# Kernel optimization log

Measured on AMD Instinct MI355X. Metric: run time of the kernel, lower is better.

## Reference

```python
import jax, jax.numpy as jnp
import numpy as np

SIGMA = 1.0
DELTA = 1.0
TOPK = 10
TOPK_HALF = 5  # int(np.around(TOPK / 2))


def l2norm(x):
    # F.normalize: x / max(||x||, 1e-12)
    n = jnp.linalg.norm(x, axis=-1, keepdims=True)
    return x / jnp.maximum(n, 1e-12)


def cdist(a, b):
    # pairwise euclidean distance with grad-safe sqrt (0 on exact-zero dists)
    d2 = (jnp.sum(a * a, axis=1)[:, None] + jnp.sum(b * b, axis=1)[None, :]
          - 2.0 * a @ b.T)
    d2 = jnp.maximum(d2, 0.0)
    return jnp.where(d2 > 0.0, jnp.sqrt(jnp.where(d2 > 0.0, d2, 1.0)), 0.0)


def rc_weights(t_emb, idx):
    # all of this is under torch.no_grad() in the original
    N = t_emb.shape[0]
    T_dist = cdist(t_emb, t_emb)
    W_P = jnp.exp(-(T_dist ** 2) / SIGMA)
    same_id = idx[:, None] == idx[None, :]
    W_P_copy = jnp.where(same_id, 1.0, W_P)
    _, topk_index = jax.lax.top_k(W_P_copy, TOPK)            # [N, k]
    topk_half_index = topk_index[:, :TOPK_HALF]               # [N, k/2]
    rows = jnp.arange(N)[:, None]
    W_NN = jnp.zeros((N, N), W_P.dtype).at[rows, topk_index].set(1.0)
    V = (((W_NN + W_NN.T) / 2.0) == 1.0).astype(W_P.dtype)    # mutual-NN graph
    # vectorized form of the per-row loop:
    # W_C_tilda[i, j] = V[i, j] * |N(i) \cap N(j)| / |N(i)|
    deg = V.sum(axis=1)                                       # |N(i)| per row
    VV = V @ V                                                # V symmetric -> (V@V)[i,j] = |N(i) cap N(j)|
    W_C_tilda = jnp.where(V > 0.0, VV / jnp.maximum(deg, 1.0)[:, None], 0.0)
    W_C_hat = W_C_tilda[topk_half_index].mean(axis=1)         # [N, N]
    W_C = (W_C_hat + W_C_hat.T) / 2.0
    W = (W_P + W_C) / 2.0
    off_diag = 1.0 - jnp.eye(N, dtype=W.dtype)
    pos_weight = W * off_diag
    neg_weight = (1.0 - W) * off_diag
    return pos_weight, neg_weight


def rc_loss(s_emb, t_emb, idx):
    s_emb = l2norm(s_emb)        # disable_mu=True
    t_emb = l2norm(t_emb)
    N = s_emb.shape[0]
    S_dist = cdist(s_emb, s_emb)
    S_dist = S_dist / S_dist.mean(axis=1, keepdims=True)
    pos_w, neg_w = rc_weights(t_emb, idx)
    pos_w = jax.lax.stop_gradient(pos_w)
    neg_w = jax.lax.stop_gradient(neg_w)
    pull = jax.nn.relu(S_dist) ** 2 * pos_w
    push = jax.nn.relu(DELTA - S_dist) ** 2 * neg_w
    return (pull.sum() + push.sum()) / (N * (N - 1))


def kl_loss(s_f, s_g):
    # disable_mu=True -> normalize both
    s_f = l2norm(s_f)
    s_g = l2norm(s_g)
    N = s_f.shape[0]
    S_dist = cdist(s_f, s_f)
    S_dist = S_dist / S_dist.mean(axis=1, keepdims=True)
    S_bg = cdist(s_g, s_g)
    S_bg = S_bg / S_bg.mean(axis=1, keepdims=True)
    log_q = jax.nn.log_softmax(-S_dist, axis=-1)
    log_p = jax.nn.log_softmax(jax.lax.stop_gradient(-S_bg), axis=-1)
    p = jnp.exp(log_p)
    return jnp.sum(p * (log_p - log_q)) / N


def setup_inputs() -> dict:
    key = jax.random.key(0)
    k1, k2, k3, k4 = jax.random.split(key, 4)
    N = 4096
    s_f = jax.random.normal(k1, (N, 512), jnp.float32)
    s_g = jax.random.normal(k2, (N, 512), jnp.float32)
    t_g = jax.random.normal(k3, (N, 1024), jnp.float32)
    idx = jax.random.randint(k4, (N,), 0, 2048, jnp.int64 if jax.config.jax_enable_x64 else jnp.int32)
    return {"s_f": s_f, "s_g": s_g, "t_g": t_g, "idx": idx}


def reference(s_f, s_g, t_g, idx):
    loss_RC_f = rc_loss(s_f, t_g, idx)
    loss_RC_g = rc_loss(s_g, t_g, idx)
    loss_RC = (loss_RC_f + loss_RC_g) / 2.0
    loss_KL = kl_loss(s_f, s_g)
    return loss_RC, loss_KL, loss_RC + loss_KL
```

## Files before the change

kernel.cpp:

```cpp
#include <hip/hip_runtime.h>
#include <hip/hip_bf16.h>

#define NN 4096
typedef unsigned short u16;
typedef __bf16 bf16x8 __attribute__((ext_vector_type(8)));
typedef float f32x4 __attribute__((ext_vector_type(4)));
typedef u16 u16x8 __attribute__((ext_vector_type(8)));

typedef const __attribute__((address_space(1))) void* gptr_t;
typedef __attribute__((address_space(3))) void* lptr_t;

__device__ inline u16 bf16bits(float v) {
    __bf16 h = (__bf16)v;
    return __builtin_bit_cast(u16, h);
}
__device__ inline float bf16val(float v) {
    __bf16 h = (__bf16)v;
    return (float)h;
}
__device__ inline float b2f(u16 b) { return __uint_as_float(((unsigned)b) << 16); }

__device__ inline float block_sum(float v, volatile float* sbuf) {
    int lane = threadIdx.x & 63, wv = threadIdx.x >> 6;
#pragma unroll
    for (int o = 32; o > 0; o >>= 1) v += __shfl_xor(v, o, 64);
    if (lane == 0) sbuf[wv] = v;
    __syncthreads();
    float r = sbuf[0] + sbuf[1] + sbuf[2] + sbuf[3];
    __syncthreads();
    return r;
}

template <int D>
__global__ void normalize_kernel(const float* __restrict__ in, u16* __restrict__ outb,
                                 float* __restrict__ ssout) {
    __shared__ float sbuf[4];
    constexpr int NV = D / 4;
    int row = blockIdx.x, tid = threadIdx.x;
    const float4* x4 = (const float4*)(in + (size_t)row * D);
    float4 v = make_float4(0.f, 0.f, 0.f, 0.f);
    if (tid < NV) v = x4[tid];
    float s = v.x * v.x + v.y * v.y + v.z * v.z + v.w * v.w;
    float tot = block_sum(s, sbuf);
    float inv = 1.0f / fmaxf(sqrtf(tot), 1e-12f);
    float sb = 0.f;
    if (tid < NV) {
        float b0 = bf16val(v.x * inv), b1 = bf16val(v.y * inv);
        float b2 = bf16val(v.z * inv), b3 = bf16val(v.w * inv);
        ushort4 o;
        o.x = bf16bits(v.x * inv);
        o.y = bf16bits(v.y * inv);
        o.z = bf16bits(v.z * inv);
        o.w = bf16bits(v.w * inv);
        ((ushort4*)(outb + (size_t)row * D))[tid] = o;
        sb = b0 * b0 + b1 * b1 + b2 * b2 + b3 * b3;
    }
    float totb = block_sum(sb, sbuf);
    if (tid == 0) ssout[row] = totb;
}

#define TS 132
__launch_bounds__(256)
__global__ void gram_merged(const u16* __restrict__ tb, const u16* __restrict__ fb,
                            const u16* __restrict__ gb, const float* __restrict__ ss_t,
                            const float* __restrict__ ss_f, const float* __restrict__ ss_g,
                            u16* __restrict__ WP, u16* __restrict__ Sf, u16* __restrict__ Sg,
                            float* __restrict__ rsf, float* __restrict__ rsg) {
    __shared__ __align__(16) u16 smem[128 * TS];

    int bid = blockIdx.x;
    int which = (bid < 528) ? 0 : (bid < 1056 ? 1 : 2);
    int lb = bid - (which == 0 ? 0 : (which == 1 ? 528 : 1056));
    int by = 0, rem = lb;
    while (rem >= 32 - by) { rem -= 32 - by; ++by; }
    int bx = by + rem;

    const u16* X = (which == 0) ? tb : (which == 1 ? fb : gb);
    const float* ss = (which == 0) ? ss_t : (which == 1 ? ss_f : ss_g);
    u16* outp = (which == 0) ? WP : (which == 1 ? Sf : Sg);
    float* rowsum = (which == 0) ? nullptr : (which == 1 ? rsf : rsg);
    const int K = (which == 0) ? 1024 : 512;
    const bool mode1 = (which != 0);

    const int tid = threadIdx.x;
    const int wv = tid >> 6, lane = tid & 63;
    const int wr = wv >> 1, wc = wv & 1;
    const int brow = by * 128, bcol = bx * 128;
    const int r = lane & 15, kc = lane >> 4;
    const int crow = lane >> 2;
    const int koff = (lane & 3) * 8;

    f32x4 acc[4][4];
#pragma unroll
    for (int mi = 0; mi < 4; ++mi)
#pragma unroll
        for (int ni = 0; ni < 4; ++ni) acc[mi][ni] = (f32x4){0.f, 0.f, 0.f, 0.f};

    auto STAGE = [&](int buf, int k0) {
#pragma unroll
        for (int cc = 0; cc < 2; ++cc) {
            int c = wv * 2 + cc;
            const u16* ga = X + (size_t)(brow + c * 16 + crow) * K + k0 + koff;
            const u16* gbp = X + (size_t)(bcol + c * 16 + crow) * K + k0 + koff;
            __builtin_amdgcn_global_load_lds((gptr_t)ga, (lptr_t)&smem[buf * 4096 + c * 512], 16, 0, 0);
            __builtin_amdgcn_global_load_lds((gptr_t)gbp, (lptr_t)&smem[8192 + buf * 4096 + c * 512], 16, 0, 0);
        }
    };

    const int NT = K / 32;
    STAGE(0, 0);
    __syncthreads();
    for (int t = 0; t < NT; ++t) {
        int cur = t & 1;
        if (t + 1 < NT) STAGE(cur ^ 1, (t + 1) * 32);

        bf16x8 af[4], bfr[4];
#pragma unroll
        for (int mi = 0; mi < 4; ++mi)
            af[mi] = *(const bf16x8*)&smem[cur * 4096 + (wr * 64 + mi * 16 + r) * 32 + kc * 8];
#pragma unroll
        for (int ni = 0; ni < 4; ++ni)
            bfr[ni] = *(const bf16x8*)&smem[8192 + cur * 4096 + (wc * 64 + ni * 16 + r) * 32 + kc * 8];
#pragma unroll
        for (int mi = 0; mi < 4; ++mi)
#pragma unroll
            for (int ni = 0; ni < 4; ++ni)
                acc[mi][ni] = __builtin_amdgcn_mfma_f32_16x16x32_bf16(af[mi], bfr[ni], acc[mi][ni], 0, 0, 0);

        __syncthreads();
    }

    u16* tile = smem;
    const int q = lane >> 4;
#pragma unroll
    for (int mi = 0; mi < 4; ++mi) {
#pragma unroll
        for (int v = 0; v < 4; ++v) {
            int rl = wr * 64 + mi * 16 + q * 4 + v;
            float ssi = ss[brow + rl];
#pragma unroll
            for (int ni = 0; ni < 4; ++ni) {
                int cl = wc * 64 + ni * 16 + r;
                float d2 = fmaxf(ssi + ss[bcol + cl] - 2.0f * acc[mi][ni][v], 0.f);
                float o = mode1 ? sqrtf(d2) : __expf(-d2);
                tile[rl * TS + cl] = bf16bits(o);
            }
        }
    }
    __syncthreads();

    {
        int rl = tid >> 1, hf = tid & 1;
        const u16* srow = &tile[rl * TS + hf * 64];
        u16* drow = outp + (size_t)(brow + rl) * NN + bcol + hf * 64;
        float rs = 0.f;
#pragma unroll
        for (int i = 0; i < 8; ++i) {
            ushort4 aa = *(const ushort4*)(srow + i * 8);
            ushort4 bb = *(const ushort4*)(srow + i * 8 + 4);
            u16x8 pk = {aa.x, aa.y, aa.z, aa.w, bb.x, bb.y, bb.z, bb.w};
            *(u16x8*)(drow + i * 8) = pk;
            if (mode1)
                rs += b2f(aa.x) + b2f(aa.y) + b2f(aa.z) + b2f(aa.w) +
                      b2f(bb.x) + b2f(bb.y) + b2f(bb.z) + b2f(bb.w);
        }
        if (mode1) {
            rs += __shfl_xor(rs, 1, 64);
            if (hf == 0) atomicAdd(&rowsum[brow + rl], rs);
        }
    }

    if (bx != by) {
        int c = tid >> 1, hf = tid & 1;
        u16* drow = outp + (size_t)(bcol + c) * NN + brow + hf * 64;
        float rs = 0.f;
#pragma unroll
        for (int s = 0; s < 8; ++s) {
            u16 g[8];
#pragma unroll
            for (int u = 0; u < 8; ++u) g[u] = tile[(hf * 64 + s * 8 + u) * TS + c];
            u16x8 pk = {g[0], g[1], g[2], g[3], g[4], g[5], g[6], g[7]};
            *(u16x8*)(drow + s * 8) = pk;
            if (mode1)
#pragma unroll
                for (int u = 0; u < 8; ++u) rs += b2f(g[u]);
        }
        if (mode1) {
            rs += __shfl_xor(rs, 1, 64);
            if (hf == 0) atomicAdd(&rowsum[bcol + c], rs);
        }
    }
}

__global__ void topk_kernel(const u16* __restrict__ WP, const int* __restrict__ idx,
                            int* __restrict__ topk) {
    __shared__ unsigned long long sred[4];
    __shared__ unsigned long long sbest;
    int row = blockIdx.x, tid = threadIdx.x;
    int myid = idx[row];
    const u16x8* W8 = (const u16x8*)(WP + (size_t)row * NN);
    const int4* idx4 = (const int4*)idx;
    unsigned key[16];
#pragma unroll
    for (int a = 0; a < 2; ++a) {
        u16x8 w = W8[a * 256 + tid];
        int4 iA = idx4[a * 512 + tid * 2];
        int4 iB = idx4[a * 512 + tid * 2 + 1];
        int ids[8] = {iA.x, iA.y, iA.z, iA.w, iB.x, iB.y, iB.z, iB.w};
#pragma unroll
        for (int c = 0; c < 8; ++c)
            key[a * 8 + c] = (ids[c] == myid) ? 0x3F800000u : (((unsigned)w[c]) << 16);
    }
    int lane = tid & 63, wv = tid >> 6;
    for (int it = 0; it < 10; ++it) {
        unsigned long long best = 0;
#pragma unroll
        for (int a = 0; a < 2; ++a)
#pragma unroll
            for (int c = 0; c < 8; ++c) {
                unsigned j = (unsigned)(a * 2048 + tid * 8 + c);
                unsigned long long pk =
                    ((unsigned long long)key[a * 8 + c] << 32) | (0xFFFFFFFFu - j);
                if (pk > best) best = pk;
            }
#pragma unroll
        for (int o = 32; o > 0; o >>= 1) {
            unsigned long long t = __shfl_xor(best, o, 64);
            if (t > best) best = t;
        }
        if (lane == 0) sred[wv] = best;
        __syncthreads();
        if (tid == 0) {
            unsigned long long b = sred[0];
            for (int w2 = 1; w2 < 4; ++w2)
                if (sred[w2] > b) b = sred[w2];
            sbest = b;
        }
        __syncthreads();
        unsigned jstar = 0xFFFFFFFFu - (unsigned)(sbest & 0xFFFFFFFFu);
        if (tid == 0) topk[row * 10 + it] = (int)jstar;
        if (((jstar >> 3) & 255u) == (unsigned)tid) {
            unsigned slot = ((jstar >> 11) << 3) | (jstar & 7u);
#pragma unroll
            for (int a = 0; a < 16; ++a)
                if ((unsigned)a == slot) key[a] = 0u;
        }
        __syncthreads();
    }
}

__global__ void mutual_kernel(const int* __restrict__ topk, int* __restrict__ nbr,
                              int* __restrict__ deg) {
    int gid = blockIdx.x * 256 + threadIdx.x;
    if (gid >= NN * 10) return;
    int i = gid / 10, a = gid - i * 10;
    int j = topk[i * 10 + a];
    bool mut = false;
#pragma unroll
    for (int b = 0; b < 10; ++b) mut = mut || (topk[j * 10 + b] == i);
    nbr[gid] = mut ? j : -1;
    if (mut) atomicAdd(&deg[i], 1);
}

__global__ void tilda_kernel(const int* __restrict__ nbr, const int* __restrict__ deg,
                             float* __restrict__ tvals) {
    int gid = blockIdx.x * 256 + threadIdx.x;
    if (gid >= NN * 10) return;
    int m = gid / 10;
    int j = nbr[gid];
    if (j < 0) { tvals[gid] = 0.f; return; }
    int am[10], aj[10];
#pragma unroll
    for (int p = 0; p < 10; ++p) am[p] = nbr[m * 10 + p];
#pragma unroll
    for (int p = 0; p < 10; ++p) aj[p] = nbr[j * 10 + p];
    int cnt = 0;
#pragma unroll
    for (int p = 0; p < 10; ++p)
#pragma unroll
        for (int qq = 0; qq < 10; ++qq)
            cnt += (am[p] >= 0 && am[p] == aj[qq]) ? 1 : 0;
    int dm = deg[m];
    float dv = (float)(dm > 1 ? dm : 1);
    tvals[gid] = (float)cnt / dv;
}

__global__ void hat_kernel(const int* __restrict__ topk, const int* __restrict__ nbr,
                           const float* __restrict__ tvals, int* __restrict__ hcols,
                           float* __restrict__ hvals) {
    int gid = blockIdx.x * 256 + threadIdx.x;
    if (gid >= NN * 5) return;
    int i = gid / 5, h = gid - i * 5;
    int m = topk[i * 10 + h];
#pragma unroll
    for (int a = 0; a < 10; ++a) {
        int j = nbr[m * 10 + a];
        int slot = i * 50 + h * 10 + a;
        hcols[slot] = j;
        hvals[slot] = (j >= 0) ? tvals[m * 10 + a] * 0.2f : 0.f;
    }
}

__global__ void fused_dense_kernel(const u16* __restrict__ Sf, const u16* __restrict__ Sg,
                                   const u16* __restrict__ WP, const float* __restrict__ rsf,
                                   const float* __restrict__ rsg, double* __restrict__ acc) {
    __shared__ float sbuf[4];
    int row = blockIdx.x, tid = threadIdx.x;
    float imf = (float)NN / rsf[row];
    float img = (float)NN / rsg[row];
    const u16x8* f8 = (const u16x8*)(Sf + (size_t)row * NN);
    const u16x8* g8 = (const u16x8*)(Sg + (size_t)row * NN);
    const u16x8* w8 = (const u16x8*)(WP + (size_t)row * NN);
    u16x8 fr[2], gr[2];
#pragma unroll
    for (int a = 0; a < 2; ++a) {
        fr[a] = f8[a * 256 + tid];
        gr[a] = g8[a * 256 + tid];
    }
    float vf[16], vg[16];
#pragma unroll
    for (int a = 0; a < 2; ++a)
#pragma unroll
        for (int c = 0; c < 8; ++c) {
            vf[a * 8 + c] = b2f(fr[a][c]) * imf;
            vg[a * 8 + c] = b2f(gr[a][c]) * img;
        }
    float ef = 0.f, eg = 0.f;
#pragma unroll
    for (int a = 0; a < 16; ++a) {
        ef += __expf(-vf[a]);
        eg += __expf(-vg[a]);
    }
    float lf = logf(block_sum(ef, sbuf));
    float lg = logf(block_sum(eg, sbuf));
    u16x8 wr2[2];
#pragma unroll
    for (int a = 0; a < 2; ++a) wr2[a] = w8[a * 256 + tid];
    float af = 0.f, ag = 0.f, akl = 0.f;
#pragma unroll
    for (int a = 0; a < 2; ++a) {
#pragma unroll
        for (int c = 0; c < 8; ++c) {
            int j = a * 2048 + tid * 8 + c;
            float wp = b2f(wr2[a][c]);
            float sf = vf[a * 8 + c], sg = vg[a * 8 + c];
            if (j != row) {
                float t = fmaxf(1.f - sf, 0.f);
                float pu = t * t;
                float gq = sf * sf - pu;
                af += pu + 0.5f * gq * wp;
                t = fmaxf(1.f - sg, 0.f);
                pu = t * t;
                gq = sg * sg - pu;
                ag += pu + 0.5f * gq * wp;
            }
            float lq = -sf - lf;
            float lp = -sg - lg;
            float pp = __expf(lp);
            akl += pp * (lp - lq);
        }
    }
    float tf = block_sum(af, sbuf);
    float tg2 = block_sum(ag, sbuf);
    float tk = block_sum(akl, sbuf);
    if (tid == 0) {
        int bank = (row & 15) * 3;
        atomicAdd(&acc[bank + 0], (double)tf);
        atomicAdd(&acc[bank + 1], (double)tg2);
        atomicAdd(&acc[bank + 2], (double)tk);
    }
}

__global__ void sparse_kernel(const u16* __restrict__ Sf, const u16* __restrict__ Sg,
                              const int* __restrict__ hcols, const float* __restrict__ hvals,
                              const float* __restrict__ rsf, const float* __restrict__ rsg,
                              double* __restrict__ acc) {
    __shared__ float sbuf[4];
    int lane = threadIdx.x & 63, wv = threadIdx.x >> 6;
    int i = blockIdx.x * 4 + wv;
    float cf = 0.f, cg = 0.f;
    if (lane < 50) {
        int j = hcols[i * 50 + lane];
        if (j >= 0 && j != i) {
            float v = hvals[i * 50 + lane];
            float imfi = (float)NN / rsf[i];
            float imgi = (float)NN / rsg[i];
            float s1 = b2f(Sf[(size_t)i * NN + j]) * imfi;
            float s2 = b2f(Sf[(size_t)j * NN + i]) * ((float)NN / rsf[j]);
            float t1 = fmaxf(1.f - s1, 0.f), t2 = fmaxf(1.f - s2, 0.f);
            cf = v * ((s1 * s1 - t1 * t1) + (s2 * s2 - t2 * t2));
            s1 = b2f(Sg[(size_t)i * NN + j]) * imgi;
            s2 = b2f(Sg[(size_t)j * NN + i]) * ((float)NN / rsg[j]);
            t1 = fmaxf(1.f - s1, 0.f);
            t2 = fmaxf(1.f - s2, 0.f);
            cg = v * ((s1 * s1 - t1 * t1) + (s2 * s2 - t2 * t2));
        }
    }
    float tf = block_sum(cf, sbuf);
    float tg = block_sum(cg, sbuf);
    if (threadIdx.x == 0) {
        int bank = (blockIdx.x & 15) * 3;
        atomicAdd(&acc[bank + 0], (double)(0.25f * tf));
        atomicAdd(&acc[bank + 1], (double)(0.25f * tg));
    }
}

__global__ void finalize_kernel(const double* __restrict__ acc, float* __restrict__ out) {
    if (threadIdx.x == 0) {
        double a0 = 0.0, a1 = 0.0, a2 = 0.0;
        for (int b = 0; b < 16; ++b) {
            a0 += acc[b * 3 + 0];
            a1 += acc[b * 3 + 1];
            a2 += acc[b * 3 + 2];
        }
        double denom = (double)NN * (double)(NN - 1);
        double rcf = a0 / denom, rcg = a1 / denom;
        double rc = 0.5 * (rcf + rcg);
        double kl = a2 / (double)NN;
        out[0] = (float)rc;
        out[1] = (float)kl;
        out[2] = (float)(rc + kl);
    }
}

extern "C" void kernel_launch(void* const* d_in, const int* in_sizes, int n_in, void* d_out,
                              int out_size, void* d_ws, size_t ws_size, hipStream_t stream) {
    const float* s_f = (const float*)d_in[0];
    const float* s_g = (const float*)d_in[1];
    const float* t_g = (const float*)d_in[2];
    const int* idx = (const int*)d_in[3];
    float* out = (float*)d_out;

    char* base = (char*)d_ws;
    size_t off = 0;
    auto alloc = [&](size_t b) {
        char* p = base + off;
        off = (off + b + 255) & ~(size_t)255;
        return p;
    };
    double* acc = (double*)alloc(16 * 3 * 8);
    float* rowsum_f = (float*)alloc(NN * 4);
    float* rowsum_g = (float*)alloc(NN * 4);
    int* deg = (int*)alloc(NN * 4);
    size_t zero_bytes = off;
    u16* tb = (u16*)alloc((size_t)NN * 1024 * 2);
    u16* fb = (u16*)alloc((size_t)NN * 512 * 2);
    u16* gb = (u16*)alloc((size_t)NN * 512 * 2);
    float* ss_t = (float*)alloc(NN * 4);
    float* ss_f = (float*)alloc(NN * 4);
    float* ss_g = (float*)alloc(NN * 4);
    u16* WP = (u16*)alloc((size_t)NN * NN * 2);
    u16* Sf = (u16*)alloc((size_t)NN * NN * 2);
    u16* Sg = (u16*)alloc((size_t)NN * NN * 2);
    int* topk = (int*)alloc(NN * 10 * 4);
    int* nbr = (int*)alloc(NN * 10 * 4);
    float* tvals = (float*)alloc(NN * 10 * 4);
    int* hcols = (int*)alloc(NN * 50 * 4);
    float* hvals = (float*)alloc(NN * 50 * 4);

    hipMemsetAsync(d_ws, 0, zero_bytes, stream);

    normalize_kernel<1024><<<NN, 256, 0, stream>>>(t_g, tb, ss_t);
    normalize_kernel<512><<<NN, 256, 0, stream>>>(s_f, fb, ss_f);
    normalize_kernel<512><<<NN, 256, 0, stream>>>(s_g, gb, ss_g);

    gram_merged<<<1584, 256, 0, stream>>>(tb, fb, gb, ss_t, ss_f, ss_g, WP, Sf, Sg,
                                          rowsum_f, rowsum_g);

    topk_kernel<<<NN, 256, 0, stream>>>(WP, idx, topk);
    mutual_kernel<<<(NN * 10 + 255) / 256, 256, 0, stream>>>(topk, nbr, deg);
    tilda_kernel<<<(NN * 10 + 255) / 256, 256, 0, stream>>>(nbr, deg, tvals);
    hat_kernel<<<(NN * 5 + 255) / 256, 256, 0, stream>>>(topk, nbr, tvals, hcols, hvals);

    fused_dense_kernel<<<NN, 256, 0, stream>>>(Sf, Sg, WP, rowsum_f, rowsum_g, acc);
    sparse_kernel<<<NN / 4, 256, 0, stream>>>(Sf, Sg, hcols, hvals, rowsum_f, rowsum_g, acc);
    finalize_kernel<<<1, 64, 0, stream>>>(acc, out);
}
```

Measured before the change: 240.6 us.

## Enlarge gram tiles to 256x256 with 1024-thread blocks and LDS transposed epilogue

The symmetric gram kernel now uses 256x256 output tiles computed by 16 waves in a 1024-thread block, so each tile loads fewer operands relative to its output and the grid drops to 408 blocks. The epilogue writes each 128x128 quadrant through LDS, and off-diagonal tiles also get a transposed copy built in LDS so the mirrored writes are contiguous instead of strided column gathers. The cost is more LDS per block, extra barriers per quadrant, and far fewer blocks, which may leave the GPU's compute units underfilled or unevenly loaded.

```diff
diff --git a/kernel.cpp b/kernel.cpp
--- a/kernel.cpp
+++ b/kernel.cpp
@@ -59,20 +59,20 @@
     if (tid == 0) ssout[row] = totb;
 }
 
-#define TS 132
-__launch_bounds__(256)
+#define TS 136
+__launch_bounds__(1024, 4)
 __global__ void gram_merged(const u16* __restrict__ tb, const u16* __restrict__ fb,
                             const u16* __restrict__ gb, const float* __restrict__ ss_t,
                             const float* __restrict__ ss_f, const float* __restrict__ ss_g,
                             u16* __restrict__ WP, u16* __restrict__ Sf, u16* __restrict__ Sg,
                             float* __restrict__ rsf, float* __restrict__ rsg) {
-    __shared__ __align__(16) u16 smem[128 * TS];
+    __shared__ __align__(16) u16 smem[34816];
 
     int bid = blockIdx.x;
-    int which = (bid < 528) ? 0 : (bid < 1056 ? 1 : 2);
-    int lb = bid - (which == 0 ? 0 : (which == 1 ? 528 : 1056));
+    int which = (bid < 136) ? 0 : (bid < 272 ? 1 : 2);
+    int lb = bid - which * 136;
     int by = 0, rem = lb;
-    while (rem >= 32 - by) { rem -= 32 - by; ++by; }
+    while (rem >= 16 - by) { rem -= 16 - by; ++by; }
     int bx = by + rem;
 
     const u16* X = (which == 0) ? tb : (which == 1 ? fb : gb);
@@ -81,11 +81,12 @@
     float* rowsum = (which == 0) ? nullptr : (which == 1 ? rsf : rsg);
     const int K = (which == 0) ? 1024 : 512;
     const bool mode1 = (which != 0);
+    const bool offdiag = (bx != by);
 
     const int tid = threadIdx.x;
     const int wv = tid >> 6, lane = tid & 63;
-    const int wr = wv >> 1, wc = wv & 1;
-    const int brow = by * 128, bcol = bx * 128;
+    const int wr = wv >> 2, wc = wv & 3;
+    const int brow = by * 256, bcol = bx * 256;
     const int r = lane & 15, kc = lane >> 4;
     const int crow = lane >> 2;
     const int koff = (lane & 3) * 8;
@@ -100,10 +101,11 @@
 #pragma unroll
         for (int cc = 0; cc < 2; ++cc) {
             int c = wv * 2 + cc;
-            const u16* ga = X + (size_t)(brow + c * 16 + crow) * K + k0 + koff;
-            const u16* gbp = X + (size_t)(bcol + c * 16 + crow) * K + k0 + koff;
-            __builtin_amdgcn_global_load_lds((gptr_t)ga, (lptr_t)&smem[buf * 4096 + c * 512], 16, 0, 0);
-            __builtin_amdgcn_global_load_lds((gptr_t)gbp, (lptr_t)&smem[8192 + buf * 4096 + c * 512], 16, 0, 0);
+            bool isB = c >= 16;
+            int c16 = isB ? c - 16 : c;
+            const u16* g = X + (size_t)((isB ? bcol : brow) + c16 * 16 + crow) * K + k0 + koff;
+            int ldsoff = (isB ? 16384 : 0) + buf * 8192 + c16 * 512;
+            __builtin_amdgcn_global_load_lds((gptr_t)g, (lptr_t)&smem[ldsoff], 16, 0, 0);
         }
     };
 
@@ -117,10 +119,10 @@
         bf16x8 af[4], bfr[4];
 #pragma unroll
         for (int mi = 0; mi < 4; ++mi)
-            af[mi] = *(const bf16x8*)&smem[cur * 4096 + (wr * 64 + mi * 16 + r) * 32 + kc * 8];
+            af[mi] = *(const bf16x8*)&smem[cur * 8192 + (wr * 64 + mi * 16 + r) * 32 + kc * 8];
 #pragma unroll
         for (int ni = 0; ni < 4; ++ni)
-            bfr[ni] = *(const bf16x8*)&smem[8192 + cur * 4096 + (wc * 64 + ni * 16 + r) * 32 + kc * 8];
+            bfr[ni] = *(const bf16x8*)&smem[16384 + cur * 8192 + (wc * 64 + ni * 16 + r) * 32 + kc * 8];
 #pragma unroll
         for (int mi = 0; mi < 4; ++mi)
 #pragma unroll
@@ -131,63 +133,70 @@
     }
 
     u16* tile = smem;
-    const int q = lane >> 4;
-#pragma unroll
-    for (int mi = 0; mi < 4; ++mi) {
-#pragma unroll
-        for (int v = 0; v < 4; ++v) {
-            int rl = wr * 64 + mi * 16 + q * 4 + v;
-            float ssi = ss[brow + rl];
-#pragma unroll
-            for (int ni = 0; ni < 4; ++ni) {
-                int cl = wc * 64 + ni * 16 + r;
-                float d2 = fmaxf(ssi + ss[bcol + cl] - 2.0f * acc[mi][ni][v], 0.f);
-                float o = mode1 ? sqrtf(d2) : __expf(-d2);
-                tile[rl * TS + cl] = bf16bits(o);
+    u16* tileT = smem + 17408;
+    const int q4 = lane >> 4;
+    const int myqr = wr >> 1, myqc = wc >> 1;
+#pragma unroll
+    for (int qr = 0; qr < 2; ++qr) {
+#pragma unroll
+        for (int qc = 0; qc < 2; ++qc) {
+            __syncthreads();
+            if (myqr == qr && myqc == qc) {
+#pragma unroll
+                for (int mi = 0; mi < 4; ++mi) {
+#pragma unroll
+                    for (int v = 0; v < 4; ++v) {
+                        int rl = (wr & 1) * 64 + mi * 16 + q4 * 4 + v;
+                        float ssi = ss[brow + qr * 128 + rl];
+#pragma unroll
+                        for (int ni = 0; ni < 4; ++ni) {
+                            int cl = (wc & 1) * 64 + ni * 16 + r;
+                            float d2 = fmaxf(ssi + ss[bcol + qc * 128 + cl] - 2.0f * acc[mi][ni][v], 0.f);
+                            float o = mode1 ? sqrtf(d2) : __expf(-d2);
+                            u16 ob = bf16bits(o);
+                            tile[rl * TS + cl] = ob;
+                            if (offdiag) tileT[cl * TS + rl] = ob;
+                        }
+                    }
+                }
             }
-        }
-    }
-    __syncthreads();
-
-    {
-        int rl = tid >> 1, hf = tid & 1;
-        const u16* srow = &tile[rl * TS + hf * 64];
-        u16* drow = outp + (size_t)(brow + rl) * NN + bcol + hf * 64;
-        float rs = 0.f;
-#pragma unroll
-        for (int i = 0; i < 8; ++i) {
-            ushort4 aa = *(const ushort4*)(srow + i * 8);
-            ushort4 bb = *(const ushort4*)(srow + i * 8 + 4);
-            u16x8 pk = {aa.x, aa.y, aa.z, aa.w, bb.x, bb.y, bb.z, bb.w};
-            *(u16x8*)(drow + i * 8) = pk;
-            if (mode1)
-                rs += b2f(aa.x) + b2f(aa.y) + b2f(aa.z) + b2f(aa.w) +
-                      b2f(bb.x) + b2f(bb.y) + b2f(bb.z) + b2f(bb.w);
-        }
-        if (mode1) {
-            rs += __shfl_xor(rs, 1, 64);
-            if (hf == 0) atomicAdd(&rowsum[brow + rl], rs);
-        }
-    }
-
-    if (bx != by) {
-        int c = tid >> 1, hf = tid & 1;
-        u16* drow = outp + (size_t)(bcol + c) * NN + brow + hf * 64;
-        float rs = 0.f;
-#pragma unroll
-        for (int s = 0; s < 8; ++s) {
-            u16 g[8];
-#pragma unroll
-            for (int u = 0; u < 8; ++u) g[u] = tile[(hf * 64 + s * 8 + u) * TS + c];
-            u16x8 pk = {g[0], g[1], g[2], g[3], g[4], g[5], g[6], g[7]};
-            *(u16x8*)(drow + s * 8) = pk;
-            if (mode1)
-#pragma unroll
-                for (int u = 0; u < 8; ++u) rs += b2f(g[u]);
-        }
-        if (mode1) {
-            rs += __shfl_xor(rs, 1, 64);
-            if (hf == 0) atomicAdd(&rowsum[bcol + c], rs);
+            __syncthreads();
+            {
+                int rl = tid >> 3, hseg = tid & 7;
+                const u16* srow = &tile[rl * TS + hseg * 16];
+                u16x8 p0 = *(const u16x8*)srow;
+                u16x8 p1 = *(const u16x8*)(srow + 8);
+                u16* drow = outp + (size_t)(brow + qr * 128 + rl) * NN + bcol + qc * 128 + hseg * 16;
+                *(u16x8*)drow = p0;
+                *(u16x8*)(drow + 8) = p1;
+                if (mode1) {
+                    float rs = 0.f;
+#pragma unroll
+                    for (int u = 0; u < 8; ++u) rs += b2f(p0[u]) + b2f(p1[u]);
+                    rs += __shfl_xor(rs, 1, 64);
+                    rs += __shfl_xor(rs, 2, 64);
+                    rs += __shfl_xor(rs, 4, 64);
+                    if ((tid & 7) == 0) atomicAdd(&rowsum[brow + qr * 128 + rl], rs);
+                }
+            }
+            if (offdiag) {
+                int cl = tid >> 3, hseg = tid & 7;
+                const u16* srow = &tileT[cl * TS + hseg * 16];
+                u16x8 p0 = *(const u16x8*)srow;
+                u16x8 p1 = *(const u16x8*)(srow + 8);
+                u16* drow = outp + (size_t)(bcol + qc * 128 + cl) * NN + brow + qr * 128 + hseg * 16;
+                *(u16x8*)drow = p0;
+                *(u16x8*)(drow + 8) = p1;
+                if (mode1) {
+                    float rs = 0.f;
+#pragma unroll
+                    for (int u = 0; u < 8; ++u) rs += b2f(p0[u]) + b2f(p1[u]);
+                    rs += __shfl_xor(rs, 1, 64);
+                    rs += __shfl_xor(rs, 2, 64);
+                    rs += __shfl_xor(rs, 4, 64);
+                    if ((tid & 7) == 0) atomicAdd(&rowsum[bcol + qc * 128 + cl], rs);
+                }
+            }
         }
     }
 }
@@ -464,7 +473,7 @@
     normalize_kernel<512><<<NN, 256, 0, stream>>>(s_f, fb, ss_f);
     normalize_kernel<512><<<NN, 256, 0, stream>>>(s_g, gb, ss_g);
 
-    gram_merged<<<1584, 256, 0, stream>>>(tb, fb, gb, ss_t, ss_f, ss_g, WP, Sf, Sg,
+    gram_merged<<<408, 1024, 0, stream>>>(tb, fb, gb, ss_t, ss_f, ss_g, WP, Sf, Sg,
                                           rowsum_f, rowsum_g);
 
     topk_kernel<<<NN, 256, 0, stream>>>(WP, idx, topk);
```

Result: slower. 292.5 us (+21.6%).

## Triple-buffer gram tile loads with explicit waitcnt and swizzle block order

Applied to the files above, without the earlier changes.

Changes the gram kernel's K-loop from double to triple buffering in LDS. Two stages are prefetched, and manual vmcnt/lgkmcnt waits with s_barrier replace __syncthreads, so global loads overlap more with MFMA work. Block indices are also remapped with a stride-66 interleave so that concurrently running blocks touch different tile rows and columns, which may change L2 locality. Shared memory grows to 24576 elements, which may reduce occupancy.

```diff
diff --git a/kernel.cpp b/kernel.cpp
--- a/kernel.cpp
+++ b/kernel.cpp
@@ -66,21 +66,23 @@
                             const float* __restrict__ ss_f, const float* __restrict__ ss_g,
                             u16* __restrict__ WP, u16* __restrict__ Sf, u16* __restrict__ Sg,
                             float* __restrict__ rsf, float* __restrict__ rsg) {
-    __shared__ __align__(16) u16 smem[128 * TS];
+    __shared__ __align__(16) u16 smem[24576];
 
     int bid = blockIdx.x;
-    int which = (bid < 528) ? 0 : (bid < 1056 ? 1 : 2);
-    int lb = bid - (which == 0 ? 0 : (which == 1 ? 528 : 1056));
-    int by = 0, rem = lb;
+    int seg = (bid < 528) ? 0 : (bid < 1056 ? 1 : 2);
+    int p = bid - seg * 528;
+    int l = (p & 7) * 66 + (p >> 3);
+    int by = 0, rem = l;
     while (rem >= 32 - by) { rem -= 32 - by; ++by; }
     int bx = by + rem;
 
-    const u16* X = (which == 0) ? tb : (which == 1 ? fb : gb);
-    const float* ss = (which == 0) ? ss_t : (which == 1 ? ss_f : ss_g);
-    u16* outp = (which == 0) ? WP : (which == 1 ? Sf : Sg);
-    float* rowsum = (which == 0) ? nullptr : (which == 1 ? rsf : rsg);
-    const int K = (which == 0) ? 1024 : 512;
-    const bool mode1 = (which != 0);
+    const u16* X = (seg == 0) ? tb : (seg == 1 ? fb : gb);
+    const float* ss = (seg == 0) ? ss_t : (seg == 1 ? ss_f : ss_g);
+    u16* outp = (seg == 0) ? WP : (seg == 1 ? Sf : Sg);
+    float* rowsum = (seg == 0) ? nullptr : (seg == 1 ? rsf : rsg);
+    const int K = (seg == 0) ? 1024 : 512;
+    const bool mode1 = (seg != 0);
+    const bool offdiag = (bx != by);
 
     const int tid = threadIdx.x;
     const int wv = tid >> 6, lane = tid & 63;
@@ -103,16 +105,19 @@
             const u16* ga = X + (size_t)(brow + c * 16 + crow) * K + k0 + koff;
             const u16* gbp = X + (size_t)(bcol + c * 16 + crow) * K + k0 + koff;
             __builtin_amdgcn_global_load_lds((gptr_t)ga, (lptr_t)&smem[buf * 4096 + c * 512], 16, 0, 0);
-            __builtin_amdgcn_global_load_lds((gptr_t)gbp, (lptr_t)&smem[8192 + buf * 4096 + c * 512], 16, 0, 0);
+            __builtin_amdgcn_global_load_lds((gptr_t)gbp, (lptr_t)&smem[12288 + buf * 4096 + c * 512], 16, 0, 0);
         }
     };
 
     const int NT = K / 32;
     STAGE(0, 0);
-    __syncthreads();
+    STAGE(1, 32);
     for (int t = 0; t < NT; ++t) {
-        int cur = t & 1;
-        if (t + 1 < NT) STAGE(cur ^ 1, (t + 1) * 32);
+        int cur = t % 3;
+        if (t == NT - 1) asm volatile("s_waitcnt vmcnt(0)" ::: "memory");
+        else             asm volatile("s_waitcnt vmcnt(4)" ::: "memory");
+        __builtin_amdgcn_sched_barrier(0);
+        __builtin_amdgcn_s_barrier();
 
         bf16x8 af[4], bfr[4];
 #pragma unroll
@@ -120,15 +125,21 @@
             af[mi] = *(const bf16x8*)&smem[cur * 4096 + (wr * 64 + mi * 16 + r) * 32 + kc * 8];
 #pragma unroll
         for (int ni = 0; ni < 4; ++ni)
-            bfr[ni] = *(const bf16x8*)&smem[8192 + cur * 4096 + (wc * 64 + ni * 16 + r) * 32 + kc * 8];
+            bfr[ni] = *(const bf16x8*)&smem[12288 + cur * 4096 + (wc * 64 + ni * 16 + r) * 32 + kc * 8];
+
+        if (t + 2 < NT) STAGE((t + 2) % 3, (t + 2) * 32);
+
+        asm volatile("s_waitcnt lgkmcnt(0)" ::: "memory");
+        __builtin_amdgcn_sched_barrier(0);
+        __builtin_amdgcn_s_barrier();
+
 #pragma unroll
         for (int mi = 0; mi < 4; ++mi)
 #pragma unroll
             for (int ni = 0; ni < 4; ++ni)
                 acc[mi][ni] = __builtin_amdgcn_mfma_f32_16x16x32_bf16(af[mi], bfr[ni], acc[mi][ni], 0, 0, 0);
-
-        __syncthreads();
-    }
+    }
+    __syncthreads();
 
     u16* tile = smem;
     const int q = lane >> 4;
@@ -170,7 +181,7 @@
         }
     }
 
-    if (bx != by) {
+    if (offdiag) {
         int c = tid >> 1, hf = tid & 1;
         u16* drow = outp + (size_t)(bcol + c) * NN + brow + hf * 64;
         float rs = 0.f;
```

Measured after the change: 229.1 us. -4.8%, faster.
